# Kernel optimization log

Measured on AMD Instinct MI355X. Metric: run time of the kernel, lower is better.

The kernel has to match this reference:

```python
import jax, jax.numpy as jnp
import numpy as np

TWO_PI = np.float32(2.0 * np.pi)
N_GABORS = 256
H = W = 512


def setup_inputs() -> dict:
    key = jax.random.key(0)
    ks = jax.random.split(key, 10)
    f32 = jnp.float32
    return {
        "grid_x": jax.random.uniform(ks[0], (H, W), dtype=f32),
        "grid_y": jax.random.uniform(ks[1], (H, W), dtype=f32),
        "u": jax.random.normal(ks[2], (N_GABORS,), dtype=f32),
        "v": jax.random.normal(ks[3], (N_GABORS,), dtype=f32),
        "theta": 2.0 * jax.random.normal(ks[4], (N_GABORS,), dtype=f32),
        "rel_sigma": 0.05 + 0.7 * jax.random.normal(ks[5], (N_GABORS,), dtype=f32),
        "rel_freq": 0.03 + 5.0 * jax.random.normal(ks[6], (N_GABORS,), dtype=f32),
        "gamma": 0.03 + 0.15 * jax.random.normal(ks[7], (N_GABORS,), dtype=f32),
        "psi": 3.0 * jax.random.normal(ks[8], (N_GABORS, 3), dtype=f32),
        "amplitude": 0.2 * jax.random.normal(ks[9], (N_GABORS, 3), dtype=f32),
    }


def reference(grid_x, grid_y, u, v, theta, rel_sigma, rel_freq, gamma, psi, amplitude):
    # Parameter range enforcement (enforce_parameter_ranges + forward clamps)
    uc = jnp.clip(u, -1.0, 1.0)
    vc = jnp.clip(v, -1.0, 1.0)
    th = jnp.clip(theta, -2.0, 2.0) * TWO_PI           # [N]
    sig = jnp.clip(rel_sigma, 1e-5, 5.0)               # [N]
    gam = jnp.clip(gamma, 1e-5, 5.0)                   # [N]
    psi_c = jnp.clip(psi, -1.0, 1.0)                   # [N,3]
    amp = jnp.clip(amplitude, 0.0, 1.0)                # [N,3]

    cr = jnp.cos(th)[:, None, None]
    sr = jnp.sin(th)[:, None, None]
    dx = grid_x[None, :, :] - uc[:, None, None]        # [N,H,W]
    dy = grid_y[None, :, :] - vc[:, None, None]
    x_rot = dx * cr + dy * sr                          # [N,H,W]
    y_rot = -dx * sr + dy * cr

    gaussian = jnp.exp(jnp.clip(
        -x_rot ** 2 / (2.0 * sig[:, None, None] ** 2)
        - y_rot ** 2 / (2.0 * gam[:, None, None] ** 2),
        -80.0, 80.0))                                  # [N,H,W]

    freq = TWO_PI / jnp.exp(rel_freq)                  # [N]
    phase = psi_c * TWO_PI                             # [N,3]
    fx = freq[:, None, None] * x_rot                   # [N,H,W]

    # cos(fx + phase) = cos(fx)cos(phase) - sin(fx)sin(phase):
    # contract the gabor dim without materializing [N,3,H,W].
    gc = gaussian * jnp.cos(fx)                        # [N,H,W]
    gs = gaussian * jnp.sin(fx)                        # [N,H,W]
    result = (jnp.einsum('nhw,nc->chw', gc, amp * jnp.cos(phase))
              - jnp.einsum('nhw,nc->chw', gs, amp * jnp.sin(phase)))  # [3,H,W]
    return jnp.clip(result, -1.0, 1.0)
```

## Files before the change

kernel.cpp:

```cpp
#include <hip/hip_runtime.h>
#include <stdint.h>

#define NG 256
#define HW (512*512)
#define NCELL 1024
#define CAP 384
#define SPILL_CAP 4096
#define NBIN 256
#define PXB (HW/NBIN)
#define TWO_PI_F 6.283185307179586f
#define L2E 1.4426950408889634f
#define INV2PI_D 0.15915494309189535
#define SKIP_THR (-16.0f)

typedef float v2f __attribute__((ext_vector_type(2)));

static __device__ __forceinline__ float clampf(float x, float lo, float hi) {
    return fminf(fmaxf(x, lo), hi);
}

static __device__ __forceinline__ void compute_consts(
    int n,
    const float* __restrict__ u, const float* __restrict__ v,
    const float* __restrict__ theta, const float* __restrict__ rel_sigma,
    const float* __restrict__ rel_freq, const float* __restrict__ gamma,
    const float* __restrict__ psi, const float* __restrict__ amplitude,
    float4& A, float4& B, float4& C, float4& D)
{
    const float uc = clampf(u[n], -1.f, 1.f);
    const float vc = clampf(v[n], -1.f, 1.f);
    const float th = clampf(theta[n], -2.f, 2.f) * TWO_PI_F;
    const float sg = clampf(rel_sigma[n], 1e-5f, 5.f);
    const float gm = clampf(gamma[n], 1e-5f, 5.f);
    const float cr = (float)::cos((double)th);
    const float sr = (float)::sin((double)th);
    const float i2s = 1.0f / (2.0f * sg * sg);
    const float i2g = 1.0f / (2.0f * gm * gm);
    const float E  = (float)::exp((double)rel_freq[n]);
    const float fq = TWO_PI_F / E;
    A = make_float4(uc, vc, cr, sr);
    B = make_float4(-(i2s * L2E), -(i2g * L2E), fq, 0.f);
    float ac[3], as[3];
    #pragma unroll
    for (int c = 0; c < 3; ++c) {
        const float ph = clampf(psi[n*3 + c], -1.f, 1.f) * TWO_PI_F;
        const float a  = clampf(amplitude[n*3 + c], 0.f, 1.f);
        ac[c] = a * (float)::cos((double)ph);
        as[c] = a * (float)::sin((double)ph);
    }
    C = make_float4(ac[0], ac[1], ac[2], 0.f);
    D = make_float4(as[0], as[1], as[2], 0.f);
}

static __device__ __forceinline__ void accum_list(
    const float4* __restrict__ base, int ngab,
    float gx, float gy, float& a0, float& a1, float& a2)
{
    const float c1f = 0.15915494309189535f;
    const float c2f = (float)(INV2PI_D - (double)0.15915494309189535f);
    for (int j = 0; j < ngab; ++j) {
        const float4 k0 = base[j];
        const float4 k1 = base[NG + j];
        const float dx = gx - k0.x;
        const float dy = gy - k0.y;
        float xr, yr;
        {
            #pragma clang fp contract(off)
            xr = dx * k0.z + dy * k0.w;
            yr = dy * k0.z - dx * k0.w;
        }
        const float e2 = fmaf(yr * yr, k1.y, xr * xr * k1.x);
        if (e2 > SKIP_THR) {
            const float g = __builtin_amdgcn_exp2f(e2);
            float fx;
            {
                #pragma clang fp contract(off)
                fx = k1.z * xr;
            }
            const float nn = __builtin_rintf(fx * c1f);
            float t = __builtin_fmaf(fx, c1f, -nn);
            t = __builtin_fmaf(fx, c2f, t);
            const float s = __builtin_amdgcn_sinf(t);
            const float c = __builtin_amdgcn_cosf(t);
            const float4 k2 = base[2*NG + j];
            const float4 k3 = base[3*NG + j];
            const float gc = g * c, gs = g * s;
            a0 = fmaf(gc, k2.x, fmaf(-gs, k3.x, a0));
            a1 = fmaf(gc, k2.y, fmaf(-gs, k3.y, a1));
            a2 = fmaf(gc, k2.z, fmaf(-gs, k3.z, a2));
        }
    }
}

__global__ __launch_bounds__(256) void gabor_bin_consts(
    const float* __restrict__ grid_x, const float* __restrict__ grid_y,
    const float* __restrict__ u, const float* __restrict__ v,
    const float* __restrict__ theta, const float* __restrict__ rel_sigma,
    const float* __restrict__ rel_freq, const float* __restrict__ gamma,
    const float* __restrict__ psi, const float* __restrict__ amplitude,
    float4* __restrict__ consts, int* __restrict__ counts,
    float4* __restrict__ bpx,
    int* __restrict__ spill, int* __restrict__ spilln)
{
    const int tid = threadIdx.x;
    if (blockIdx.x == NBIN) {
        float4 A, B, C, D;
        compute_consts(tid, u, v, theta, rel_sigma, rel_freq, gamma, psi,
                       amplitude, A, B, C, D);
        consts[tid] = A; consts[NG+tid] = B;
        consts[2*NG+tid] = C; consts[3*NG+tid] = D;
        return;
    }
    __shared__ int hist[NCELL];
    __shared__ int base[NCELL];
    #pragma unroll
    for (int i = 0; i < NCELL/256; ++i) hist[i*256 + tid] = 0;
    __syncthreads();

    uint32_t rec[PXB/256];
    float px[PXB/256], py[PXB/256];
    const int p0 = blockIdx.x * PXB;
    #pragma unroll
    for (int i = 0; i < PXB/256; ++i) {
        const int p = p0 + i*256 + tid;
        const float x = grid_x[p], y = grid_y[p];
        px[i] = x; py[i] = y;
        int ix = (int)(x * 32.0f); ix = min(max(ix, 0), 31);
        int iy = (int)(y * 32.0f); iy = min(max(iy, 0), 31);
        const int cell = iy*32 + ix;
        const int lr = atomicAdd(&hist[cell], 1);
        rec[i] = ((uint32_t)cell << 11) | (uint32_t)lr;
    }
    __syncthreads();
    #pragma unroll
    for (int i = 0; i < NCELL/256; ++i) {
        const int c = i*256 + tid;
        const int h = hist[c];
        base[c] = (h > 0) ? atomicAdd(&counts[c], h) : 0;
    }
    __syncthreads();
    #pragma unroll
    for (int i = 0; i < PXB/256; ++i) {
        const int p = p0 + i*256 + tid;
        const int cell = (int)(rec[i] >> 11);
        const int g = base[cell] + (int)(rec[i] & 0x7FFu);
        if (g < CAP) {
            bpx[cell*CAP + g] =
                make_float4(__int_as_float(p), px[i], py[i], 0.f);
        } else {
            const int t2 = atomicAdd(spilln, 1);
            if (t2 < SPILL_CAP) spill[t2] = p;
        }
    }
}

__global__ __launch_bounds__(256) void gabor_render(
    const float4* __restrict__ consts, const int* __restrict__ counts,
    const float4* __restrict__ bpx,
    const int* __restrict__ spill, const int* __restrict__ spilln,
    const float* __restrict__ grid_x, const float* __restrict__ grid_y,
    float* __restrict__ out)
{
    __shared__ float4 pkUV[NG/2];
    __shared__ float4 pkROT[NG/2];
    __shared__ float4 pkSG[NG/2];
    __shared__ float2 pkFQ[NG/2];
    __shared__ float4 pkAMP[3][NG/2];
    __shared__ float4 c2A[NG], c2B[NG], c2C[NG], c2D[NG];
    __shared__ int s_wb1[4], s_wb2[4];

    const int cell = blockIdx.x;
    const int tid = threadIdx.x;
    const float cxc = ((cell & 31) + 0.5f) * 0.03125f;
    const float cyc = ((cell >> 5) + 0.5f) * 0.03125f;

    {
        const float4 A = consts[tid];
        const float4 B = consts[NG + tid];
        const float4 C = consts[2*NG + tid];
        const float4 D = consts[3*NG + tid];
        const float dx = cxc - A.x, dy = cyc - A.y;
        const float xrc = dx * A.z + dy * A.w;
        const float yrc = dy * A.z - dx * A.w;
        const float R = 0.0222f;
        const float axr = fabsf(xrc), ayr = fabsf(yrc);
        const float xl = fmaxf(axr - R, 0.f), yl = fmaxf(ayr - R, 0.f);
        const float xh = axr + R,            yh = ayr + R;
        const float e2max = xl*xl*B.x + yl*yl*B.y;
        const float e2min = xh*xh*B.x + yh*yh*B.y;
        const bool nz = (C.x != 0.f) | (C.y != 0.f) | (C.z != 0.f) |
                        (D.x != 0.f) | (D.y != 0.f) | (D.z != 0.f);
        const bool act = (e2max > SKIP_THR) && nz;
        const bool g1  = act && (e2min > SKIP_THR);
        const bool g2  = act && !g1;
        const unsigned long long m1 = __ballot(g1);
        const unsigned long long m2 = __ballot(g2);
        const int lane = tid & 63, w = tid >> 6;
        if (lane == 0) { s_wb1[w] = __popcll(m1); s_wb2[w] = __popcll(m2); }
        __syncthreads();
        int b1 = 0, b2 = 0;
        #pragma unroll
        for (int i = 0; i < 4; ++i) {
            b1 += (i < w) ? s_wb1[i] : 0;
            b2 += (i < w) ? s_wb2[i] : 0;
        }
        const unsigned long long lm = (1ull << lane) - 1ull;
        if (g1) {
            const int pos = b1 + __popcll(m1 & lm);
            const int q = pos >> 1, h = pos & 1;
            if (h == 0) {
                pkUV[q].x = A.x;  pkUV[q].z = A.y;
                pkROT[q].x = A.z; pkROT[q].z = A.w;
                pkSG[q].x = B.x;  pkSG[q].z = B.y;
                pkFQ[q].x = B.z;
                pkAMP[0][q].x = C.x; pkAMP[0][q].z = D.x;
                pkAMP[1][q].x = C.y; pkAMP[1][q].z = D.y;
                pkAMP[2][q].x = C.z; pkAMP[2][q].z = D.z;
            } else {
                pkUV[q].y = A.x;  pkUV[q].w = A.y;
                pkROT[q].y = A.z; pkROT[q].w = A.w;
                pkSG[q].y = B.x;  pkSG[q].w = B.y;
                pkFQ[q].y = B.z;
                pkAMP[0][q].y = C.x; pkAMP[0][q].w = D.x;
                pkAMP[1][q].y = C.y; pkAMP[1][q].w = D.y;
                pkAMP[2][q].y = C.z; pkAMP[2][q].w = D.z;
            }
        }
        if (g2) {
            const int pos = b2 + __popcll(m2 & lm);
            c2A[pos] = A; c2B[pos] = B; c2C[pos] = C; c2D[pos] = D;
        }
        __syncthreads();
    }
    const int n1 = s_wb1[0] + s_wb1[1] + s_wb1[2] + s_wb1[3];
    const int n2 = s_wb2[0] + s_wb2[1] + s_wb2[2] + s_wb2[3];
    if (tid == 0 && (n1 & 1)) {
        const int q = n1 >> 1;
        pkUV[q].y = 0.f;  pkUV[q].w = 0.f;
        pkROT[q].y = 1.f; pkROT[q].w = 0.f;
        pkSG[q].y = 0.f;  pkSG[q].w = 0.f;
        pkFQ[q].y = 0.f;
        pkAMP[0][q].y = 0.f; pkAMP[0][q].w = 0.f;
        pkAMP[1][q].y = 0.f; pkAMP[1][q].w = 0.f;
        pkAMP[2][q].y = 0.f; pkAMP[2][q].w = 0.f;
    }
    __syncthreads();
    const int n1p = (n1 + 1) >> 1;

    const float c1f = 0.15915494309189535f;
    const float c2f = (float)(INV2PI_D - (double)0.15915494309189535f);
    const v2f c1p = {c1f, c1f};
    const v2f c2p = {c2f, c2f};
    const int cnt = min(counts[cell], CAP);
    const int sb = cell * CAP;
    for (int i = tid; i < cnt; i += 256) {
        const float4 pxk = bpx[sb + i];
        const int   p  = __float_as_int(pxk.x);
        const float gx = pxk.y, gy = pxk.z;
        const v2f gxp = {gx, gx}, gyp = {gy, gy};
        v2f A0 = {0.f, 0.f}, A1 = {0.f, 0.f}, A2 = {0.f, 0.f};
        #pragma unroll 4
        for (int q = 0; q < n1p; ++q) {
            const float4 tuv = pkUV[q];
            const float4 trt = pkROT[q];
            const float4 tsg = pkSG[q];
            const float2 tfq = pkFQ[q];
            const v2f up  = {tuv.x, tuv.y}, vp  = {tuv.z, tuv.w};
            const v2f crp = {trt.x, trt.y}, srp = {trt.z, trt.w};
            const v2f isp = {tsg.x, tsg.y}, igp = {tsg.z, tsg.w};
            const v2f fqp = {tfq.x, tfq.y};
            const v2f dx = gxp - up;
            const v2f dy = gyp - vp;
            v2f xr, yr;
            {
                #pragma clang fp contract(off)
                xr = dx * crp + dy * srp;
                yr = dy * crp - dx * srp;
            }
            const v2f e2 = (xr * xr) * isp + (yr * yr) * igp;
            const v2f g = { __builtin_amdgcn_exp2f(e2.x),
                            __builtin_amdgcn_exp2f(e2.y) };
            v2f fx;
            {
                #pragma clang fp contract(off)
                fx = fqp * xr;
            }
            const v2f r1 = fx * c1p;
            const v2f nn = { __builtin_rintf(r1.x), __builtin_rintf(r1.y) };
            v2f t = __builtin_elementwise_fma(fx, c1p, -nn);
            t = __builtin_elementwise_fma(fx, c2p, t);
            const v2f s = { __builtin_amdgcn_sinf(t.x),
                            __builtin_amdgcn_sinf(t.y) };
            const v2f c = { __builtin_amdgcn_cosf(t.x),
                            __builtin_amdgcn_cosf(t.y) };
            const v2f gc = g * c, gs = g * s;
            const float4 am0 = pkAMP[0][q];
            const float4 am1 = pkAMP[1][q];
            const float4 am2 = pkAMP[2][q];
            const v2f ac0 = {am0.x, am0.y}, as0 = {am0.z, am0.w};
            const v2f ac1 = {am1.x, am1.y}, as1 = {am1.z, am1.w};
            const v2f ac2 = {am2.x, am2.y}, as2 = {am2.z, am2.w};
            A0 = __builtin_elementwise_fma(gc, ac0,
                 __builtin_elementwise_fma(-gs, as0, A0));
            A1 = __builtin_elementwise_fma(gc, ac1,
                 __builtin_elementwise_fma(-gs, as1, A1));
            A2 = __builtin_elementwise_fma(gc, ac2,
                 __builtin_elementwise_fma(-gs, as2, A2));
        }
        float a0 = A0.x + A0.y, a1 = A1.x + A1.y, a2 = A2.x + A2.y;
        for (int j = 0; j < n2; ++j) {
            const float4 k0 = c2A[j];
            const float4 k1 = c2B[j];
            const float dx = gx - k0.x;
            const float dy = gy - k0.y;
            float xr, yr;
            {
                #pragma clang fp contract(off)
                xr = dx * k0.z + dy * k0.w;
                yr = dy * k0.z - dx * k0.w;
            }
            const float e2 = fmaf(yr * yr, k1.y, xr * xr * k1.x);
            if (e2 > SKIP_THR) {
                const float g = __builtin_amdgcn_exp2f(e2);
                float fx;
                {
                    #pragma clang fp contract(off)
                    fx = k1.z * xr;
                }
                const float nn = __builtin_rintf(fx * c1f);
                float t = __builtin_fmaf(fx, c1f, -nn);
                t = __builtin_fmaf(fx, c2f, t);
                const float s = __builtin_amdgcn_sinf(t);
                const float c = __builtin_amdgcn_cosf(t);
                const float4 k2 = c2C[j];
                const float4 k3 = c2D[j];
                const float gc = g * c, gs = g * s;
                a0 = fmaf(gc, k2.x, fmaf(-gs, k3.x, a0));
                a1 = fmaf(gc, k2.y, fmaf(-gs, k3.y, a1));
                a2 = fmaf(gc, k2.z, fmaf(-gs, k3.z, a2));
            }
        }
        out[p]        = clampf(a0, -1.f, 1.f);
        out[HW + p]   = clampf(a1, -1.f, 1.f);
        out[2*HW + p] = clampf(a2, -1.f, 1.f);
    }

    if (cell == 0) {
        const int sc = min(*spilln, SPILL_CAP);
        for (int i = tid; i < sc; i += 256) {
            const int p = spill[i];
            const float gx = grid_x[p], gy = grid_y[p];
            float a0 = 0.f, a1 = 0.f, a2 = 0.f;
            accum_list(consts, NG, gx, gy, a0, a1, a2);
            out[p]        = clampf(a0, -1.f, 1.f);
            out[HW + p]   = clampf(a1, -1.f, 1.f);
            out[2*HW + p] = clampf(a2, -1.f, 1.f);
        }
    }
}

__global__ __launch_bounds__(256) void gabor_consts_kernel(
    const float* __restrict__ u, const float* __restrict__ v,
    const float* __restrict__ theta, const float* __restrict__ rel_sigma,
    const float* __restrict__ rel_freq, const float* __restrict__ gamma,
    const float* __restrict__ psi, const float* __restrict__ amplitude,
    float4* __restrict__ ws)
{
    const int n = threadIdx.x;
    float4 A, B, C, D;
    compute_consts(n, u, v, theta, rel_sigma, rel_freq, gamma, psi, amplitude,
                   A, B, C, D);
    ws[n] = A; ws[NG + n] = B; ws[2*NG + n] = C; ws[3*NG + n] = D;
}

__global__ __launch_bounds__(256) void gabor_fwd_ws(
    const float4* __restrict__ ws,
    const float* __restrict__ grid_x, const float* __restrict__ grid_y,
    float* __restrict__ out)
{
    __shared__ float4 cs[4 * NG];
    const int tid = threadIdx.x;
    cs[tid]        = ws[tid];
    cs[tid + NG]   = ws[tid + NG];
    cs[tid + 2*NG] = ws[tid + 2*NG];
    cs[tid + 3*NG] = ws[tid + 3*NG];
    __syncthreads();
    const int p = blockIdx.x * 256 + tid;
    const float gx = grid_x[p], gy = grid_y[p];
    float a0 = 0.f, a1 = 0.f, a2 = 0.f;
    accum_list(cs, NG, gx, gy, a0, a1, a2);
    out[p]        = clampf(a0, -1.f, 1.f);
    out[HW + p]   = clampf(a1, -1.f, 1.f);
    out[2*HW + p] = clampf(a2, -1.f, 1.f);
}

__global__ __launch_bounds__(256) void gabor_fwd_fused(
    const float* __restrict__ grid_x, const float* __restrict__ grid_y,
    const float* __restrict__ u, const float* __restrict__ v,
    const float* __restrict__ theta, const float* __restrict__ rel_sigma,
    const float* __restrict__ rel_freq, const float* __restrict__ gamma,
    const float* __restrict__ psi, const float* __restrict__ amplitude,
    float* __restrict__ out)
{
    __shared__ float4 cs[4 * NG];
    const int tid = threadIdx.x;
    {
        float4 A, B, C, D;
        compute_consts(tid, u, v, theta, rel_sigma, rel_freq, gamma, psi,
                       amplitude, A, B, C, D);
        cs[tid] = A; cs[tid + NG] = B; cs[tid + 2*NG] = C; cs[tid + 3*NG] = D;
    }
    __syncthreads();
    const int p = blockIdx.x * 256 + tid;
    const float gx = grid_x[p], gy = grid_y[p];
    float a0 = 0.f, a1 = 0.f, a2 = 0.f;
    accum_list(cs, NG, gx, gy, a0, a1, a2);
    out[p]        = clampf(a0, -1.f, 1.f);
    out[HW + p]   = clampf(a1, -1.f, 1.f);
    out[2*HW + p] = clampf(a2, -1.f, 1.f);
}

extern "C" void kernel_launch(void* const* d_in, const int* in_sizes, int n_in,
                              void* d_out, int out_size, void* d_ws, size_t ws_size,
                              hipStream_t stream) {
    const float* grid_x    = (const float*)d_in[0];
    const float* grid_y    = (const float*)d_in[1];
    const float* u         = (const float*)d_in[2];
    const float* v         = (const float*)d_in[3];
    const float* theta     = (const float*)d_in[4];
    const float* rel_sigma = (const float*)d_in[5];
    const float* rel_freq  = (const float*)d_in[6];
    const float* gamma     = (const float*)d_in[7];
    const float* psi       = (const float*)d_in[8];
    const float* amplitude = (const float*)d_in[9];
    float* out = (float*)d_out;

    const size_t OFF_CONSTS = 0;
    const size_t OFF_COUNTS = 16384;
    const size_t OFF_SPN    = 20480;
    const size_t OFF_SPILL  = 20736;
    const size_t OFF_BPX    = 37120;
    const size_t NEED       = 6328576;

    char* w = (char*)d_ws;

    if (ws_size >= NEED) {
        float4* consts = (float4*)(w + OFF_CONSTS);
        int*    counts = (int*)(w + OFF_COUNTS);
        int*    spn    = (int*)(w + OFF_SPN);
        int*    spill  = (int*)(w + OFF_SPILL);
        float4* bpx    = (float4*)(w + OFF_BPX);

        hipMemsetAsync(w + OFF_COUNTS, 0, 4096 + 256, stream);
        gabor_bin_consts<<<NBIN + 1, 256, 0, stream>>>(
            grid_x, grid_y, u, v, theta, rel_sigma, rel_freq, gamma,
            psi, amplitude, consts, counts, bpx, spill, spn);
        gabor_render<<<NCELL, 256, 0, stream>>>(
            consts, counts, bpx, spill, spn, grid_x, grid_y, out);
    } else if (ws_size >= 4u * NG * sizeof(float4)) {
        float4* ws = (float4*)d_ws;
        gabor_consts_kernel<<<1, NG, 0, stream>>>(
            u, v, theta, rel_sigma, rel_freq, gamma, psi, amplitude, ws);
        gabor_fwd_ws<<<HW / 256, 256, 0, stream>>>(ws, grid_x, grid_y, out);
    } else {
        gabor_fwd_fused<<<HW / 256, 256, 0, stream>>>(
            grid_x, grid_y, u, v, theta, rel_sigma, rel_freq, gamma,
            psi, amplitude, out);
    }
}
```

Measured before the change: 33.20 us.

## Split render blocks across pixel chunks and gabor halves with shared-memory reduction

The render grid doubles so that each cell is handled by two blocks, each taking half the binned pixels. Inside a block, the two 128-thread halves each sum over half of the active gabor list and combine their partial sums through shared memory before the clamp and store. The separate per-pixel skip path for partially covered gabors is dropped, so every active gabor now goes through the packed pair loop with no early skip. This should raise parallelism and occupancy (launch bounds now request 6 waves) but adds barriers, duplicates the per-block constant culling, and does more exp/sin work on gabors that previously could be skipped per pixel.

Result: no change. 33.56 us (+1.1%).

```diff
diff --git a/kernel.cpp b/kernel.cpp
--- a/kernel.cpp
+++ b/kernel.cpp
@@ -154,7 +154,7 @@
     }
 }
 
-__global__ __launch_bounds__(256) void gabor_render(
+__global__ __launch_bounds__(256, 6) void gabor_render(
     const float4* __restrict__ consts, const int* __restrict__ counts,
     const float4* __restrict__ bpx,
     const int* __restrict__ spill, const int* __restrict__ spilln,
@@ -166,10 +166,10 @@
     __shared__ float4 pkSG[NG/2];
     __shared__ float2 pkFQ[NG/2];
     __shared__ float4 pkAMP[3][NG/2];
-    __shared__ float4 c2A[NG], c2B[NG], c2C[NG], c2D[NG];
-    __shared__ int s_wb1[4], s_wb2[4];
-
-    const int cell = blockIdx.x;
+    __shared__ float  red[128*3];
+    __shared__ int s_wb[4];
+
+    const int cell = blockIdx.x >> 1, chunk = blockIdx.x & 1;
     const int tid = threadIdx.x;
     const float cxc = ((cell & 31) + 0.5f) * 0.03125f;
     const float cyc = ((cell >> 5) + 0.5f) * 0.03125f;
@@ -183,30 +183,21 @@
         const float xrc = dx * A.z + dy * A.w;
         const float yrc = dy * A.z - dx * A.w;
         const float R = 0.0222f;
-        const float axr = fabsf(xrc), ayr = fabsf(yrc);
-        const float xl = fmaxf(axr - R, 0.f), yl = fmaxf(ayr - R, 0.f);
-        const float xh = axr + R,            yh = ayr + R;
+        const float xl = fmaxf(fabsf(xrc) - R, 0.f);
+        const float yl = fmaxf(fabsf(yrc) - R, 0.f);
         const float e2max = xl*xl*B.x + yl*yl*B.y;
-        const float e2min = xh*xh*B.x + yh*yh*B.y;
         const bool nz = (C.x != 0.f) | (C.y != 0.f) | (C.z != 0.f) |
                         (D.x != 0.f) | (D.y != 0.f) | (D.z != 0.f);
         const bool act = (e2max > SKIP_THR) && nz;
-        const bool g1  = act && (e2min > SKIP_THR);
-        const bool g2  = act && !g1;
-        const unsigned long long m1 = __ballot(g1);
-        const unsigned long long m2 = __ballot(g2);
+        const unsigned long long m = __ballot(act);
         const int lane = tid & 63, w = tid >> 6;
-        if (lane == 0) { s_wb1[w] = __popcll(m1); s_wb2[w] = __popcll(m2); }
+        if (lane == 0) s_wb[w] = __popcll(m);
         __syncthreads();
-        int b1 = 0, b2 = 0;
+        int b = 0;
         #pragma unroll
-        for (int i = 0; i < 4; ++i) {
-            b1 += (i < w) ? s_wb1[i] : 0;
-            b2 += (i < w) ? s_wb2[i] : 0;
-        }
-        const unsigned long long lm = (1ull << lane) - 1ull;
-        if (g1) {
-            const int pos = b1 + __popcll(m1 & lm);
+        for (int i = 0; i < 4; ++i) b += (i < w) ? s_wb[i] : 0;
+        if (act) {
+            const int pos = b + __popcll(m & ((1ull << lane) - 1ull));
             const int q = pos >> 1, h = pos & 1;
             if (h == 0) {
                 pkUV[q].x = A.x;  pkUV[q].z = A.y;
@@ -226,14 +217,9 @@
                 pkAMP[2][q].y = C.z; pkAMP[2][q].w = D.z;
             }
         }
-        if (g2) {
-            const int pos = b2 + __popcll(m2 & lm);
-            c2A[pos] = A; c2B[pos] = B; c2C[pos] = C; c2D[pos] = D;
-        }
         __syncthreads();
     }
-    const int n1 = s_wb1[0] + s_wb1[1] + s_wb1[2] + s_wb1[3];
-    const int n2 = s_wb2[0] + s_wb2[1] + s_wb2[2] + s_wb2[3];
+    const int n1 = s_wb[0] + s_wb[1] + s_wb[2] + s_wb[3];
     if (tid == 0 && (n1 & 1)) {
         const int q = n1 >> 1;
         pkUV[q].y = 0.f;  pkUV[q].w = 0.f;
@@ -246,6 +232,11 @@
     }
     __syncthreads();
     const int n1p = (n1 + 1) >> 1;
+    const int split = n1p >> 1;
+    const int half = tid >> 7;
+    const int l128 = tid & 127;
+    const int qa = half ? split : 0;
+    const int qb = half ? n1p   : split;
 
     const float c1f = 0.15915494309189535f;
     const float c2f = (float)(INV2PI_D - (double)0.15915494309189535f);
@@ -253,99 +244,86 @@
     const v2f c2p = {c2f, c2f};
     const int cnt = min(counts[cell], CAP);
     const int sb = cell * CAP;
-    for (int i = tid; i < cnt; i += 256) {
-        const float4 pxk = bpx[sb + i];
-        const int   p  = __float_as_int(pxk.x);
-        const float gx = pxk.y, gy = pxk.z;
-        const v2f gxp = {gx, gx}, gyp = {gy, gy};
-        v2f A0 = {0.f, 0.f}, A1 = {0.f, 0.f}, A2 = {0.f, 0.f};
-        #pragma unroll 4
-        for (int q = 0; q < n1p; ++q) {
-            const float4 tuv = pkUV[q];
-            const float4 trt = pkROT[q];
-            const float4 tsg = pkSG[q];
-            const float2 tfq = pkFQ[q];
-            const v2f up  = {tuv.x, tuv.y}, vp  = {tuv.z, tuv.w};
-            const v2f crp = {trt.x, trt.y}, srp = {trt.z, trt.w};
-            const v2f isp = {tsg.x, tsg.y}, igp = {tsg.z, tsg.w};
-            const v2f fqp = {tfq.x, tfq.y};
-            const v2f dx = gxp - up;
-            const v2f dy = gyp - vp;
-            v2f xr, yr;
-            {
-                #pragma clang fp contract(off)
-                xr = dx * crp + dy * srp;
-                yr = dy * crp - dx * srp;
-            }
-            const v2f e2 = (xr * xr) * isp + (yr * yr) * igp;
-            const v2f g = { __builtin_amdgcn_exp2f(e2.x),
-                            __builtin_amdgcn_exp2f(e2.y) };
-            v2f fx;
-            {
-                #pragma clang fp contract(off)
-                fx = fqp * xr;
-            }
-            const v2f r1 = fx * c1p;
-            const v2f nn = { __builtin_rintf(r1.x), __builtin_rintf(r1.y) };
-            v2f t = __builtin_elementwise_fma(fx, c1p, -nn);
-            t = __builtin_elementwise_fma(fx, c2p, t);
-            const v2f s = { __builtin_amdgcn_sinf(t.x),
-                            __builtin_amdgcn_sinf(t.y) };
-            const v2f c = { __builtin_amdgcn_cosf(t.x),
-                            __builtin_amdgcn_cosf(t.y) };
-            const v2f gc = g * c, gs = g * s;
-            const float4 am0 = pkAMP[0][q];
-            const float4 am1 = pkAMP[1][q];
-            const float4 am2 = pkAMP[2][q];
-            const v2f ac0 = {am0.x, am0.y}, as0 = {am0.z, am0.w};
-            const v2f ac1 = {am1.x, am1.y}, as1 = {am1.z, am1.w};
-            const v2f ac2 = {am2.x, am2.y}, as2 = {am2.z, am2.w};
-            A0 = __builtin_elementwise_fma(gc, ac0,
-                 __builtin_elementwise_fma(-gs, as0, A0));
-            A1 = __builtin_elementwise_fma(gc, ac1,
-                 __builtin_elementwise_fma(-gs, as1, A1));
-            A2 = __builtin_elementwise_fma(gc, ac2,
-                 __builtin_elementwise_fma(-gs, as2, A2));
-        }
-        float a0 = A0.x + A0.y, a1 = A1.x + A1.y, a2 = A2.x + A2.y;
-        for (int j = 0; j < n2; ++j) {
-            const float4 k0 = c2A[j];
-            const float4 k1 = c2B[j];
-            const float dx = gx - k0.x;
-            const float dy = gy - k0.y;
-            float xr, yr;
-            {
-                #pragma clang fp contract(off)
-                xr = dx * k0.z + dy * k0.w;
-                yr = dy * k0.z - dx * k0.w;
-            }
-            const float e2 = fmaf(yr * yr, k1.y, xr * xr * k1.x);
-            if (e2 > SKIP_THR) {
-                const float g = __builtin_amdgcn_exp2f(e2);
-                float fx;
+    const int h0   = (cnt + 1) >> 1;
+    const int base = chunk ? h0  : 0;
+    const int lim  = chunk ? cnt : h0;
+    const int iters = (lim - base + 127) >> 7;
+    for (int k = 0; k < iters; ++k) {
+        const int i = base + k*128 + l128;
+        const bool have = i < lim;
+        float a0 = 0.f, a1 = 0.f, a2 = 0.f;
+        int p = 0;
+        if (have) {
+            const float4 pxk = bpx[sb + i];
+            p = __float_as_int(pxk.x);
+            const float gx = pxk.y, gy = pxk.z;
+            const v2f gxp = {gx, gx}, gyp = {gy, gy};
+            v2f A0 = {0.f, 0.f}, A1 = {0.f, 0.f}, A2 = {0.f, 0.f};
+            #pragma unroll 2
+            for (int q = qa; q < qb; ++q) {
+                const float4 tuv = pkUV[q];
+                const float4 trt = pkROT[q];
+                const float4 tsg = pkSG[q];
+                const float2 tfq = pkFQ[q];
+                const v2f up  = {tuv.x, tuv.y}, vp  = {tuv.z, tuv.w};
+                const v2f crp = {trt.x, trt.y}, srp = {trt.z, trt.w};
+                const v2f isp = {tsg.x, tsg.y}, igp = {tsg.z, tsg.w};
+                const v2f fqp = {tfq.x, tfq.y};
+                const v2f dx = gxp - up;
+                const v2f dy = gyp - vp;
+                v2f xr, yr;
                 {
                     #pragma clang fp contract(off)
-                    fx = k1.z * xr;
+                    xr = dx * crp + dy * srp;
+                    yr = dy * crp - dx * srp;
                 }
-                const float nn = __builtin_rintf(fx * c1f);
-                float t = __builtin_fmaf(fx, c1f, -nn);
-                t = __builtin_fmaf(fx, c2f, t);
-                const float s = __builtin_amdgcn_sinf(t);
-                const float c = __builtin_amdgcn_cosf(t);
-                const float4 k2 = c2C[j];
-                const float4 k3 = c2D[j];
-                const float gc = g * c, gs = g * s;
-                a0 = fmaf(gc, k2.x, fmaf(-gs, k3.x, a0));
-                a1 = fmaf(gc, k2.y, fmaf(-gs, k3.y, a1));
-                a2 = fmaf(gc, k2.z, fmaf(-gs, k3.z, a2));
+                const v2f e2 = (xr * xr) * isp + (yr * yr) * igp;
+                const v2f g = { __builtin_amdgcn_exp2f(e2.x),
+                                __builtin_amdgcn_exp2f(e2.y) };
+                v2f fx;
+                {
+                    #pragma clang fp contract(off)
+                    fx = fqp * xr;
+                }
+                const v2f r1 = fx * c1p;
+                const v2f nn = { __builtin_rintf(r1.x), __builtin_rintf(r1.y) };
+                v2f t = __builtin_elementwise_fma(fx, c1p, -nn);
+                t = __builtin_elementwise_fma(fx, c2p, t);
+                const v2f s = { __builtin_amdgcn_sinf(t.x),
+                                __builtin_amdgcn_sinf(t.y) };
+                const v2f c = { __builtin_amdgcn_cosf(t.x),
+                                __builtin_amdgcn_cosf(t.y) };
+                const v2f gc = g * c, gs = g * s;
+                const float4 am0 = pkAMP[0][q];
+                const float4 am1 = pkAMP[1][q];
+                const float4 am2 = pkAMP[2][q];
+                const v2f ac0 = {am0.x, am0.y}, as0 = {am0.z, am0.w};
+                const v2f ac1 = {am1.x, am1.y}, as1 = {am1.z, am1.w};
+                const v2f ac2 = {am2.x, am2.y}, as2 = {am2.z, am2.w};
+                A0 = __builtin_elementwise_fma(gc, ac0,
+                     __builtin_elementwise_fma(-gs, as0, A0));
+                A1 = __builtin_elementwise_fma(gc, ac1,
+                     __builtin_elementwise_fma(-gs, as1, A1));
+                A2 = __builtin_elementwise_fma(gc, ac2,
+                     __builtin_elementwise_fma(-gs, as2, A2));
             }
-        }
-        out[p]        = clampf(a0, -1.f, 1.f);
-        out[HW + p]   = clampf(a1, -1.f, 1.f);
-        out[2*HW + p] = clampf(a2, -1.f, 1.f);
-    }
-
-    if (cell == 0) {
+            a0 = A0.x + A0.y; a1 = A1.x + A1.y; a2 = A2.x + A2.y;
+        }
+        __syncthreads();
+        if (half && have) {
+            red[l128*3 + 0] = a0;
+            red[l128*3 + 1] = a1;
+            red[l128*3 + 2] = a2;
+        }
+        __syncthreads();
+        if (!half && have) {
+            out[p]        = clampf(a0 + red[l128*3 + 0], -1.f, 1.f);
+            out[HW + p]   = clampf(a1 + red[l128*3 + 1], -1.f, 1.f);
+            out[2*HW + p] = clampf(a2 + red[l128*3 + 2], -1.f, 1.f);
+        }
+    }
+
+    if (blockIdx.x == 0) {
         const int sc = min(*spilln, SPILL_CAP);
         for (int i = tid; i < sc; i += 256) {
             const int p = spill[i];
@@ -455,7 +433,7 @@
         gabor_bin_consts<<<NBIN + 1, 256, 0, stream>>>(
             grid_x, grid_y, u, v, theta, rel_sigma, rel_freq, gamma,
             psi, amplitude, consts, counts, bpx, spill, spn);
-        gabor_render<<<NCELL, 256, 0, stream>>>(
+        gabor_render<<<2*NCELL, 256, 0, stream>>>(
             consts, counts, bpx, spill, spn, grid_x, grid_y, out);
     } else if (ws_size >= 4u * NG * sizeof(float4)) {
         float4* ws = (float4*)d_ws;
```
